# Kernel optimization log

Measured on AMD Instinct MI355X. Metric: run time of the kernel, lower is better.

## Reference

```python
import jax, jax.numpy as jnp
import numpy as np

D_HEAD = 64
SCALE = 1.0 / (D_HEAD ** 0.5)
MASK_VALUE = -1e9


def setup_inputs() -> dict:
    key = jax.random.key(0)
    kq, kk, kv, km = jax.random.split(key, 4)
    B, H, S, D = 2, 12, 2048, D_HEAD
    Q = jax.random.normal(kq, (B, H, S, D), dtype=jnp.float32)
    K = jax.random.normal(kk, (B, H, S, D), dtype=jnp.float32)
    V = jax.random.normal(kv, (B, H, S, D), dtype=jnp.float32)
    attn_mask = jax.random.randint(km, (B, 1, S, S), 0, 2).astype(bool)
    return {"Q": Q, "K": K, "V": V, "attn_mask": attn_mask}


def reference(Q, K, V, attn_mask):
    # scores: [B,H,S,S]
    scores = jnp.einsum('bhqd,bhkd->bhqk', Q, K) * SCALE
    scores = jnp.where(attn_mask, MASK_VALUE, scores)
    attn_prob = jax.nn.softmax(scores, axis=-1)
    # dropout p=0.0 (eval mode) -> identity
    context = jnp.einsum('bhqk,bhkd->bhqd', attn_prob, V)
    return (context, attn_prob)
```

## Files before the change

### kernel.cpp

```cpp
#include <hip/hip_runtime.h>
#include <hip/hip_bf16.h>
#include <math.h>

#define B_SZ   2
#define NH     12
#define S_LEN  2048
#define D_HD   64
#define NQ_EL  ((size_t)B_SZ * NH * S_LEN * D_HD)

typedef __attribute__((ext_vector_type(8))) __bf16 bf16x8;
typedef __attribute__((ext_vector_type(4))) float  f32x4;

__device__ __forceinline__ int detect_mask_mode64(const void* mask) {
  const int lane = threadIdx.x & 63;
  unsigned v = ((const unsigned*)mask)[lane];
  if (__ballot(v <= 1u) == ~0ull) return 0;
  if (__ballot(v == 0u || v == 0x3f800000u) == ~0ull) return 2;
  unsigned h0 = v & 0xFFFFu, h1 = v >> 16;
  bool okb = (h0 == 0u || h0 == 0x3f80u) && (h1 == 0u || h1 == 0x3f80u);
  if (__ballot(okb) == ~0ull) return 3;
  return 1;
}

__device__ __forceinline__ bool mask_at(const void* mask, int mode, size_t idx) {
  if (mode == 0) return ((const int*)mask)[idx] != 0;
  if (mode == 1) return ((const unsigned char*)mask)[idx] != 0;
  if (mode == 2) return ((const float*)mask)[idx] != 0.0f;
  return ((const unsigned short*)mask)[idx] != 0;
}

__global__ __launch_bounds__(256)
void build_bits_kernel(const void* __restrict__ mask, unsigned* __restrict__ bits) {
  const int mode = detect_mask_mode64(mask);
  const size_t i = (size_t)blockIdx.x * 256 + threadIdx.x;
  const bool m = mask_at(mask, mode, i);
  const unsigned long long bal = __ballot(m);
  const int lane = threadIdx.x & 63;
  if (lane == 0)       bits[i >> 5] = (unsigned)bal;
  else if (lane == 32) bits[i >> 5] = (unsigned)(bal >> 32);
}

__global__ __launch_bounds__(256)
void convert_kernel(const float* __restrict__ Q, const float* __restrict__ K,
                    const float* __restrict__ V,
                    __bf16* __restrict__ Qb, __bf16* __restrict__ Kb,
                    __bf16* __restrict__ Vb) {
  const size_t nvec = NQ_EL / 4;
  for (size_t vi = (size_t)blockIdx.x * 256 + threadIdx.x; vi < 3 * nvec;
       vi += (size_t)gridDim.x * 256) {
    const int seg = vi < nvec ? 0 : (vi < 2 * nvec ? 1 : 2);
    const size_t li = vi - (size_t)seg * nvec;
    const float* src = seg == 0 ? Q : (seg == 1 ? K : V);
    __bf16* dst = seg == 0 ? Qb : (seg == 1 ? Kb : Vb);
    const float scale = seg == 0 ? 0.125f : 1.0f;
    float4 a = ((const float4*)src)[li];
    __bf16 o0 = (__bf16)(a.x * scale), o1 = (__bf16)(a.y * scale);
    __bf16 o2 = (__bf16)(a.z * scale), o3 = (__bf16)(a.w * scale);
    ((ushort4*)dst)[li] = (ushort4){
        __builtin_bit_cast(unsigned short, o0), __builtin_bit_cast(unsigned short, o1),
        __builtin_bit_cast(unsigned short, o2), __builtin_bit_cast(unsigned short, o3)};
  }
}

__device__ __forceinline__ bf16x8 ld8s(const __bf16* p, float) {
  return *(const bf16x8*)p;
}
__device__ __forceinline__ bf16x8 ld8s(const float* p, float scale) {
  const float4 a = *(const float4*)p;
  const float4 b = *(const float4*)(p + 4);
  bf16x8 r;
  r[0] = (__bf16)(a.x * scale); r[1] = (__bf16)(a.y * scale);
  r[2] = (__bf16)(a.z * scale); r[3] = (__bf16)(a.w * scale);
  r[4] = (__bf16)(b.x * scale); r[5] = (__bf16)(b.y * scale);
  r[6] = (__bf16)(b.z * scale); r[7] = (__bf16)(b.w * scale);
  return r;
}

template<typename T, bool USE_BITS, bool PRESCALED>
__global__ __launch_bounds__(512)
void attn_kernel(const T* __restrict__ Qg, const T* __restrict__ Kg,
                 const T* __restrict__ Vg, const void* __restrict__ mask,
                 const unsigned* __restrict__ mbits, float* __restrict__ out_ctx)
{
  float* out_p = out_ctx + NQ_EL;

  const int flat = blockIdx.x + blockIdx.y * gridDim.x;
  const int wf   = (flat & 7) * 96 + (flat >> 3);
  const int qt   = wf & 31;
  const int bh   = wf >> 5;
  const int b    = bh / NH;

  const int tid  = threadIdx.x;
  const int lane = tid & 63;
  const int w    = tid >> 6;
  const int qw   = w & 3;
  const int kh   = w >> 2;
  const int qbase = qt * 64 + qw * 16;
  const int col  = lane & 15;
  const int g    = lane >> 4;
  const int qrow_r0 = qbase + g * 4;
  const int k0   = kh * (S_LEN / 2);

  const size_t mrow0 = (size_t)b * S_LEN * S_LEN;
  int mmode = 0;
  if constexpr (!USE_BITS) mmode = detect_mask_mode64(mask);

  const size_t qoff = ((size_t)bh * S_LEN + qbase + col) * D_HD + g * 8;
  const bf16x8 a0 = ld8s(Qg + qoff,      PRESCALED ? 1.0f : 0.125f);
  const bf16x8 a1 = ld8s(Qg + qoff + 32, PRESCALED ? 1.0f : 0.125f);

  __shared__ __align__(16) __bf16 vt[2][D_HD][40];
  __shared__ __align__(16) __bf16 pbuf[8][16][40];
  __shared__ float lsh[8][16];
  __shared__ float csum[4][16][66];

  float lsum[4] = {0.f, 0.f, 0.f, 0.f};
  for (int kc = k0; kc < k0 + S_LEN / 2; kc += 32) {
    unsigned mw[4];
    if constexpr (USE_BITS) {
#pragma unroll
      for (int r = 0; r < 4; r++)
        mw[r] = mbits[(mrow0 >> 5) + (size_t)(qrow_r0 + r) * (S_LEN / 32) + (kc >> 5)];
    }
#pragma unroll
    for (int sub = 0; sub < 2; sub++) {
      const int kb = kc + sub * 16;
      const size_t koff = ((size_t)bh * S_LEN + kb + col) * D_HD + g * 8;
      bf16x8 b0 = ld8s(Kg + koff,      1.0f);
      bf16x8 b1 = ld8s(Kg + koff + 32, 1.0f);
      f32x4 acc = {0.f, 0.f, 0.f, 0.f};
      acc = __builtin_amdgcn_mfma_f32_16x16x32_bf16(a0, b0, acc, 0, 0, 0);
      acc = __builtin_amdgcn_mfma_f32_16x16x32_bf16(a1, b1, acc, 0, 0, 0);
#pragma unroll
      for (int r = 0; r < 4; r++) {
        bool msk;
        if constexpr (USE_BITS) msk = (mw[r] >> (sub * 16 + col)) & 1;
        else msk = mask_at(mask, mmode,
                           mrow0 + (size_t)(qrow_r0 + r) * S_LEN + kb + col);
        float s = msk ? -1e9f : acc[r];
        lsum[r] += __expf(s);
      }
    }
  }
#pragma unroll
  for (int r = 0; r < 4; r++) {
    lsum[r] += __shfl_xor(lsum[r], 1);
    lsum[r] += __shfl_xor(lsum[r], 2);
    lsum[r] += __shfl_xor(lsum[r], 4);
    lsum[r] += __shfl_xor(lsum[r], 8);
  }
  if (col == 0) {
#pragma unroll
    for (int r = 0; r < 4; r++) lsh[w][g * 4 + r] = lsum[r];
  }
  __syncthreads();
  float inv_l[4];
#pragma unroll
  for (int r = 0; r < 4; r++)
    inv_l[r] = 1.0f / (lsum[r] + lsh[w ^ 4][g * 4 + r]);

  f32x4 cacc[4];
#pragma unroll
  for (int dt = 0; dt < 4; dt++) cacc[dt] = (f32x4){0.f, 0.f, 0.f, 0.f};

  float* prow = out_p + (size_t)bh * S_LEN * S_LEN;

  for (int it = 0; it < S_LEN / 64; ++it) {
    __syncthreads();
    {
      const int kh2 = tid >> 8;
      const int rem = tid & 255;
      const int kk  = rem >> 3;
      const int d0  = (rem & 7) * 8;
      bf16x8 vv = ld8s(
          Vg + ((size_t)bh * S_LEN + kh2 * (S_LEN / 2) + it * 32 + kk) * D_HD + d0,
          1.0f);
#pragma unroll
      for (int j = 0; j < 8; j++) vt[kh2][d0 + j][kk] = vv[j];
    }

    const int kc = k0 + it * 32;
    unsigned mw[4];
    if constexpr (USE_BITS) {
#pragma unroll
      for (int r = 0; r < 4; r++)
        mw[r] = mbits[(mrow0 >> 5) + (size_t)(qrow_r0 + r) * (S_LEN / 32) + (kc >> 5)];
    }
#pragma unroll
    for (int sub = 0; sub < 2; sub++) {
      const int kb = kc + sub * 16;
      const size_t koff = ((size_t)bh * S_LEN + kb + col) * D_HD + g * 8;
      bf16x8 b0 = ld8s(Kg + koff,      1.0f);
      bf16x8 b1 = ld8s(Kg + koff + 32, 1.0f);
      f32x4 acc = {0.f, 0.f, 0.f, 0.f};
      acc = __builtin_amdgcn_mfma_f32_16x16x32_bf16(a0, b0, acc, 0, 0, 0);
      acc = __builtin_amdgcn_mfma_f32_16x16x32_bf16(a1, b1, acc, 0, 0, 0);
#pragma unroll
      for (int r = 0; r < 4; r++) {
        bool msk;
        if constexpr (USE_BITS) msk = (mw[r] >> (sub * 16 + col)) & 1;
        else msk = mask_at(mask, mmode,
                           mrow0 + (size_t)(qrow_r0 + r) * S_LEN + kb + col);
        float s = msk ? -1e9f : acc[r];
        float p = __expf(s) * inv_l[r];
        prow[(size_t)(qrow_r0 + r) * S_LEN + kb + col] = p;
        pbuf[w][g * 4 + r][sub * 16 + col] = (__bf16)p;
      }
    }
    __syncthreads();

    bf16x8 pfrag = *(const bf16x8*)&pbuf[w][col][g * 8];
#pragma unroll
    for (int dt = 0; dt < 4; dt++) {
      bf16x8 vfrag = *(const bf16x8*)&vt[kh][dt * 16 + col][g * 8];
      cacc[dt] = __builtin_amdgcn_mfma_f32_16x16x32_bf16(pfrag, vfrag, cacc[dt], 0, 0, 0);
    }
  }

  __syncthreads();
  if (kh == 1) {
#pragma unroll
    for (int dt = 0; dt < 4; dt++)
#pragma unroll
      for (int r = 0; r < 4; r++)
        csum[qw][g * 4 + r][dt * 16 + col] = cacc[dt][r];
  }
  __syncthreads();
  if (kh == 0) {
#pragma unroll
    for (int dt = 0; dt < 4; dt++)
#pragma unroll
      for (int r = 0; r < 4; r++)
        out_ctx[((size_t)bh * S_LEN + qrow_r0 + r) * D_HD + dt * 16 + col] =
            cacc[dt][r] + csum[qw][g * 4 + r][dt * 16 + col];
  }
}

extern "C" void kernel_launch(void* const* d_in, const int* in_sizes, int n_in,
                              void* d_out, int out_size, void* d_ws, size_t ws_size,
                              hipStream_t stream) {
  const float* Q = (const float*)d_in[0];
  const float* K = (const float*)d_in[1];
  const float* V = (const float*)d_in[2];
  const void* mask = d_in[3];
  float* out = (float*)d_out;

  const size_t mask_elems = (size_t)B_SZ * S_LEN * S_LEN;
  const size_t off_bits = 256;
  const size_t off_q = off_bits + mask_elems / 8;
  const size_t off_k = off_q + NQ_EL * 2;
  const size_t off_v = off_k + NQ_EL * 2;
  const size_t need  = off_v + NQ_EL * 2;
  dim3 grid(S_LEN / 64, B_SZ * NH);

  if (ws_size >= need) {
    unsigned* bits = (unsigned*)((char*)d_ws + off_bits);
    __bf16* Qb = (__bf16*)((char*)d_ws + off_q);
    __bf16* Kb = (__bf16*)((char*)d_ws + off_k);
    __bf16* Vb = (__bf16*)((char*)d_ws + off_v);
    build_bits_kernel<<<(unsigned)(mask_elems / 256), 256, 0, stream>>>(mask, bits);
    convert_kernel<<<2048, 256, 0, stream>>>(Q, K, V, Qb, Kb, Vb);
    attn_kernel<__bf16, true, true><<<grid, 512, 0, stream>>>(
        Qb, Kb, Vb, mask, bits, out);
  } else if (ws_size >= off_q) {
    unsigned* bits = (unsigned*)((char*)d_ws + off_bits);
    build_bits_kernel<<<(unsigned)(mask_elems / 256), 256, 0, stream>>>(mask, bits);
    attn_kernel<float, true, false><<<grid, 512, 0, stream>>>(
        Q, K, V, mask, bits, out);
  } else {
    attn_kernel<float, false, false><<<grid, 512, 0, stream>>>(
        Q, K, V, mask, nullptr, out);
  }
}
```

Baseline: 280.4 us.

## Transpose the QK MFMA so each lane owns a query row, with vector prob stores

The K and Q operands of the score MFMA are swapped, so each lane now holds four consecutive keys of a single query row. That lets each lane load one mask word per step, write the probability tile with float4 stores, and build the P·V A-fragment directly in registers, which removes the pbuf shared-memory round trip. V staging is double-buffered so only one barrier per iteration remains. The risks are a changed register and LDS-access pattern for the V fragment reads and extra shared memory for the second V buffer.

New measurement: 293.3 us. 1.05x slower.

```diff
diff --git a/kernel.cpp b/kernel.cpp
--- a/kernel.cpp
+++ b/kernel.cpp
@@ -9,6 +9,7 @@
 #define NQ_EL  ((size_t)B_SZ * NH * S_LEN * D_HD)
 
 typedef __attribute__((ext_vector_type(8))) __bf16 bf16x8;
+typedef __attribute__((ext_vector_type(4))) __bf16 bf16x4;
 typedef __attribute__((ext_vector_type(4))) float  f32x4;
 
 __device__ __forceinline__ int detect_mask_mode64(const void* mask) {
@@ -98,126 +99,114 @@
   const int qbase = qt * 64 + qw * 16;
   const int col  = lane & 15;
   const int g    = lane >> 4;
-  const int qrow_r0 = qbase + g * 4;
+  const int q    = qbase + col;
   const int k0   = kh * (S_LEN / 2);
 
-  const size_t mrow0 = (size_t)b * S_LEN * S_LEN;
   int mmode = 0;
   if constexpr (!USE_BITS) mmode = detect_mask_mode64(mask);
-
-  const size_t qoff = ((size_t)bh * S_LEN + qbase + col) * D_HD + g * 8;
-  const bf16x8 a0 = ld8s(Qg + qoff,      PRESCALED ? 1.0f : 0.125f);
-  const bf16x8 a1 = ld8s(Qg + qoff + 32, PRESCALED ? 1.0f : 0.125f);
-
-  __shared__ __align__(16) __bf16 vt[2][D_HD][40];
-  __shared__ __align__(16) __bf16 pbuf[8][16][40];
+  const size_t mrow  = (size_t)b * S_LEN * S_LEN;
+  const size_t mbase = ((size_t)b * S_LEN + q) * (S_LEN / 32);
+
+  const size_t qoff = ((size_t)bh * S_LEN + q) * D_HD + g * 8;
+  const bf16x8 bq0 = ld8s(Qg + qoff,      PRESCALED ? 1.0f : 0.125f);
+  const bf16x8 bq1 = ld8s(Qg + qoff + 32, PRESCALED ? 1.0f : 0.125f);
+
+  float lsum = 0.f;
+#pragma unroll 2
+  for (int kc = k0; kc < k0 + S_LEN / 2; kc += 32) {
+    unsigned mw = 0;
+    if constexpr (USE_BITS) mw = mbits[mbase + (kc >> 5)];
+#pragma unroll
+    for (int sub = 0; sub < 2; ++sub) {
+      const int kb = kc + sub * 16;
+      const size_t koff = ((size_t)bh * S_LEN + kb + col) * D_HD + g * 8;
+      bf16x8 ak0 = ld8s(Kg + koff,      1.0f);
+      bf16x8 ak1 = ld8s(Kg + koff + 32, 1.0f);
+      f32x4 acc = {0.f, 0.f, 0.f, 0.f};
+      acc = __builtin_amdgcn_mfma_f32_16x16x32_bf16(ak0, bq0, acc, 0, 0, 0);
+      acc = __builtin_amdgcn_mfma_f32_16x16x32_bf16(ak1, bq1, acc, 0, 0, 0);
+#pragma unroll
+      for (int r = 0; r < 4; ++r) {
+        bool msk;
+        if constexpr (USE_BITS) msk = (mw >> (sub * 16 + g * 4 + r)) & 1;
+        else msk = mask_at(mask, mmode, mrow + (size_t)q * S_LEN + kb + g * 4 + r);
+        lsum += msk ? 0.f : __expf(acc[r]);
+      }
+    }
+  }
+  lsum += __shfl_xor(lsum, 16);
+  lsum += __shfl_xor(lsum, 32);
+
+  __shared__ __align__(16) __bf16 vt[2][2][D_HD][36];
   __shared__ float lsh[8][16];
   __shared__ float csum[4][16][66];
 
-  float lsum[4] = {0.f, 0.f, 0.f, 0.f};
-  for (int kc = k0; kc < k0 + S_LEN / 2; kc += 32) {
-    unsigned mw[4];
-    if constexpr (USE_BITS) {
-#pragma unroll
-      for (int r = 0; r < 4; r++)
-        mw[r] = mbits[(mrow0 >> 5) + (size_t)(qrow_r0 + r) * (S_LEN / 32) + (kc >> 5)];
-    }
-#pragma unroll
-    for (int sub = 0; sub < 2; sub++) {
+  if (lane < 16) lsh[w][col] = lsum;
+
+  auto stage = [&](int it_, int buf_) {
+    const int kh2 = tid >> 8;
+    const int rem = tid & 255;
+    const int kk  = rem >> 3;
+    const int d0  = (rem & 7) * 8;
+    bf16x8 vv = ld8s(
+        Vg + ((size_t)bh * S_LEN + kh2 * (S_LEN / 2) + it_ * 32 + kk) * D_HD + d0,
+        1.0f);
+#pragma unroll
+    for (int j = 0; j < 8; j++) vt[buf_][kh2][d0 + j][kk] = vv[j];
+  };
+  stage(0, 0);
+  __syncthreads();
+  const float inv_l = 1.0f / (lsum + lsh[w ^ 4][col]);
+
+  f32x4 cacc[4];
+#pragma unroll
+  for (int dt = 0; dt < 4; dt++) cacc[dt] = (f32x4){0.f, 0.f, 0.f, 0.f};
+
+  float* prow = out_p + (size_t)bh * S_LEN * S_LEN + (size_t)q * S_LEN;
+
+  for (int it = 0; it < S_LEN / 64; ++it) {
+    const int cur = it & 1;
+    if (it < 31) stage(it + 1, cur ^ 1);
+
+    const int kc = k0 + it * 32;
+    unsigned mw = 0;
+    if constexpr (USE_BITS) mw = mbits[mbase + (kc >> 5)];
+
+    float p[8];
+#pragma unroll
+    for (int sub = 0; sub < 2; ++sub) {
       const int kb = kc + sub * 16;
       const size_t koff = ((size_t)bh * S_LEN + kb + col) * D_HD + g * 8;
-      bf16x8 b0 = ld8s(Kg + koff,      1.0f);
-      bf16x8 b1 = ld8s(Kg + koff + 32, 1.0f);
+      bf16x8 ak0 = ld8s(Kg + koff,      1.0f);
+      bf16x8 ak1 = ld8s(Kg + koff + 32, 1.0f);
       f32x4 acc = {0.f, 0.f, 0.f, 0.f};
-      acc = __builtin_amdgcn_mfma_f32_16x16x32_bf16(a0, b0, acc, 0, 0, 0);
-      acc = __builtin_amdgcn_mfma_f32_16x16x32_bf16(a1, b1, acc, 0, 0, 0);
-#pragma unroll
-      for (int r = 0; r < 4; r++) {
+      acc = __builtin_amdgcn_mfma_f32_16x16x32_bf16(ak0, bq0, acc, 0, 0, 0);
+      acc = __builtin_amdgcn_mfma_f32_16x16x32_bf16(ak1, bq1, acc, 0, 0, 0);
+#pragma unroll
+      for (int r = 0; r < 4; ++r) {
         bool msk;
-        if constexpr (USE_BITS) msk = (mw[r] >> (sub * 16 + col)) & 1;
-        else msk = mask_at(mask, mmode,
-                           mrow0 + (size_t)(qrow_r0 + r) * S_LEN + kb + col);
-        float s = msk ? -1e9f : acc[r];
-        lsum[r] += __expf(s);
+        if constexpr (USE_BITS) msk = (mw >> (sub * 16 + g * 4 + r)) & 1;
+        else msk = mask_at(mask, mmode, mrow + (size_t)q * S_LEN + kb + g * 4 + r);
+        p[sub * 4 + r] = msk ? 0.f : __expf(acc[r]) * inv_l;
       }
+      float4 st = {p[sub * 4 + 0], p[sub * 4 + 1], p[sub * 4 + 2], p[sub * 4 + 3]};
+      *(float4*)(prow + kb + g * 4) = st;
     }
-  }
-#pragma unroll
-  for (int r = 0; r < 4; r++) {
-    lsum[r] += __shfl_xor(lsum[r], 1);
-    lsum[r] += __shfl_xor(lsum[r], 2);
-    lsum[r] += __shfl_xor(lsum[r], 4);
-    lsum[r] += __shfl_xor(lsum[r], 8);
-  }
-  if (col == 0) {
-#pragma unroll
-    for (int r = 0; r < 4; r++) lsh[w][g * 4 + r] = lsum[r];
-  }
-  __syncthreads();
-  float inv_l[4];
-#pragma unroll
-  for (int r = 0; r < 4; r++)
-    inv_l[r] = 1.0f / (lsum[r] + lsh[w ^ 4][g * 4 + r]);
-
-  f32x4 cacc[4];
-#pragma unroll
-  for (int dt = 0; dt < 4; dt++) cacc[dt] = (f32x4){0.f, 0.f, 0.f, 0.f};
-
-  float* prow = out_p + (size_t)bh * S_LEN * S_LEN;
-
-  for (int it = 0; it < S_LEN / 64; ++it) {
-    __syncthreads();
-    {
-      const int kh2 = tid >> 8;
-      const int rem = tid & 255;
-      const int kk  = rem >> 3;
-      const int d0  = (rem & 7) * 8;
-      bf16x8 vv = ld8s(
-          Vg + ((size_t)bh * S_LEN + kh2 * (S_LEN / 2) + it * 32 + kk) * D_HD + d0,
-          1.0f);
-#pragma unroll
-      for (int j = 0; j < 8; j++) vt[kh2][d0 + j][kk] = vv[j];
-    }
-
-    const int kc = k0 + it * 32;
-    unsigned mw[4];
-    if constexpr (USE_BITS) {
-#pragma unroll
-      for (int r = 0; r < 4; r++)
-        mw[r] = mbits[(mrow0 >> 5) + (size_t)(qrow_r0 + r) * (S_LEN / 32) + (kc >> 5)];
-    }
-#pragma unroll
-    for (int sub = 0; sub < 2; sub++) {
-      const int kb = kc + sub * 16;
-      const size_t koff = ((size_t)bh * S_LEN + kb + col) * D_HD + g * 8;
-      bf16x8 b0 = ld8s(Kg + koff,      1.0f);
-      bf16x8 b1 = ld8s(Kg + koff + 32, 1.0f);
-      f32x4 acc = {0.f, 0.f, 0.f, 0.f};
-      acc = __builtin_amdgcn_mfma_f32_16x16x32_bf16(a0, b0, acc, 0, 0, 0);
-      acc = __builtin_amdgcn_mfma_f32_16x16x32_bf16(a1, b1, acc, 0, 0, 0);
-#pragma unroll
-      for (int r = 0; r < 4; r++) {
-        bool msk;
-        if constexpr (USE_BITS) msk = (mw[r] >> (sub * 16 + col)) & 1;
-        else msk = mask_at(mask, mmode,
-                           mrow0 + (size_t)(qrow_r0 + r) * S_LEN + kb + col);
-        float s = msk ? -1e9f : acc[r];
-        float p = __expf(s) * inv_l[r];
-        prow[(size_t)(qrow_r0 + r) * S_LEN + kb + col] = p;
-        pbuf[w][g * 4 + r][sub * 16 + col] = (__bf16)p;
-      }
+    bf16x8 pa;
+#pragma unroll
+    for (int e = 0; e < 8; e++) pa[e] = (__bf16)p[e];
+
+#pragma unroll
+    for (int dt = 0; dt < 4; dt++) {
+      const __bf16* vrow = &vt[cur][kh][dt * 16 + col][0];
+      bf16x4 lo = *(const bf16x4*)(vrow + g * 4);
+      bf16x4 hi = *(const bf16x4*)(vrow + 16 + g * 4);
+      bf16x8 vf = __builtin_shufflevector(lo, hi, 0, 1, 2, 3, 4, 5, 6, 7);
+      cacc[dt] = __builtin_amdgcn_mfma_f32_16x16x32_bf16(pa, vf, cacc[dt], 0, 0, 0);
     }
     __syncthreads();
-
-    bf16x8 pfrag = *(const bf16x8*)&pbuf[w][col][g * 8];
-#pragma unroll
-    for (int dt = 0; dt < 4; dt++) {
-      bf16x8 vfrag = *(const bf16x8*)&vt[kh][dt * 16 + col][g * 8];
-      cacc[dt] = __builtin_amdgcn_mfma_f32_16x16x32_bf16(pfrag, vfrag, cacc[dt], 0, 0, 0);
-    }
-  }
-
-  __syncthreads();
+  }
+
   if (kh == 1) {
 #pragma unroll
     for (int dt = 0; dt < 4; dt++)
@@ -231,7 +220,7 @@
     for (int dt = 0; dt < 4; dt++)
 #pragma unroll
       for (int r = 0; r < 4; r++)
-        out_ctx[((size_t)bh * S_LEN + qrow_r0 + r) * D_HD + dt * 16 + col] =
+        out_ctx[((size_t)bh * S_LEN + qbase + g * 4 + r) * D_HD + dt * 16 + col] =
             cacc[dt][r] + csum[qw][g * 4 + r][dt * 16 + col];
   }
 }
```
